# Kernel tuning notes

Hardware: AMD Instinct MI355X
Metric: run time of the kernel (lower is better)

The kernel has to match this reference:

```python
import jax, jax.numpy as jnp
import numpy as np

K = 3  # conv1d kernel size
PAD = (K - 1) // 2


def _conv1d_1ch(x, w, b):
    # x: (B, 1, C), w: (1, 1, K), b: (1,)  -- torch Conv1d cross-correlation
    c = x.shape[-1]
    xp = jnp.pad(x, ((0, 0), (0, 0), (PAD, PAD)))
    y = sum(w[0, 0, k] * xp[:, :, k:k + c] for k in range(K))
    return y + b[0]


def setup_inputs() -> dict:
    key = jax.random.key(0)
    ks = jax.random.split(key, 13)
    B, C, H, W, E = 8, 256, 48, 48, 64
    s = lambda fan: 1.0 / np.sqrt(fan)
    return {
        "feature": jax.random.normal(ks[0], (B, C, H, W), jnp.float32),
        "wq1": jax.random.normal(ks[1], (1, 1, K), jnp.float32) * s(K),
        "bq1": jax.random.normal(ks[2], (1,), jnp.float32) * s(K),
        "wk1": jax.random.normal(ks[3], (1, 1, K), jnp.float32) * s(K),
        "bk1": jax.random.normal(ks[4], (1,), jnp.float32) * s(K),
        "wq2": jax.random.normal(ks[5], (E, C), jnp.float32) * s(C),
        "bq2": jax.random.normal(ks[6], (E,), jnp.float32) * s(C),
        "wk2": jax.random.normal(ks[7], (E, C), jnp.float32) * s(C),
        "bk2": jax.random.normal(ks[8], (E,), jnp.float32) * s(C),
        "wv2": jax.random.normal(ks[9], (E, C), jnp.float32) * s(C),
        "bv2": jax.random.normal(ks[10], (E,), jnp.float32) * s(C),
        "watt": jax.random.normal(ks[11], (C, E), jnp.float32) * s(E),
        "batt": jax.random.normal(ks[12], (C,), jnp.float32) * s(E),
    }


def reference(feature, wq1, bq1, wk1, bk1, wq2, bq2, wk2, bk2, wv2, bv2, watt, batt):
    b, c, h, w = feature.shape
    hw = h * w

    # ---- Global Channel Attention ----
    gap = jnp.mean(feature, axis=(2, 3)).reshape(b, 1, c)
    query = jax.nn.sigmoid(_conv1d_1ch(gap, wq1, bq1))  # (b,1,c)
    key_ = jax.nn.sigmoid(_conv1d_1ch(gap, wk1, bk1))   # (b,1,c)
    att_c = key_[:, 0, :, None] * query[:, 0, None, :]  # (b,c,c) = K^T Q
    att_c = jax.nn.softmax(att_c, axis=1)               # softmax over dim=1
    value = feature.reshape(b, hw, c)                   # raw reshape, as in torch
    gc = jnp.matmul(value, att_c).reshape(b, c, h, w)   # raw reshape back

    # ---- Global Spatial Attention ----
    q = (jnp.einsum('bchw,ec->behw', feature, wq2) + bq2[None, :, None, None]).reshape(b, -1, hw)
    k = (jnp.einsum('bchw,ec->behw', feature, wk2) + bk2[None, :, None, None]).reshape(b, -1, hw)
    v = (jnp.einsum('bchw,ec->behw', feature, wv2) + bv2[None, :, None, None]).reshape(b, -1, hw)
    att_s = jnp.einsum('bei,bej->bij', k, q)            # (b,hw,hw)
    att_s = jax.nn.softmax(att_s, axis=2)
    gs = jnp.einsum('bei,bij->bej', v, att_s).reshape(b, -1, h, w)  # (b,e,h,w)
    gs = jnp.einsum('behw,ce->bchw', gs, watt) + batt[None, :, None, None]

    # ---- Gated combination ----
    feature_gc = feature * gc
    return feature_gc * gs + feature_gc
```

## Files before the change

### kernel.cpp

```cpp
#include <hip/hip_runtime.h>

#define B_ 8
#define C_ 256
#define HW_ 2304
#define E_ 64
#define SB_ (C_*HW_)

typedef unsigned short u16;
typedef __attribute__((ext_vector_type(8))) __bf16 bf16x8;
typedef __attribute__((ext_vector_type(4))) float f32x4;
#define MFMA16(a,b,c) __builtin_amdgcn_mfma_f32_16x16x32_bf16(a,b,c,0,0,0)

#define LDS_FENCE() do { asm volatile("s_waitcnt lgkmcnt(0)" ::: "memory"); \
                         __builtin_amdgcn_sched_barrier(0); } while(0)

static __device__ inline u16 f2bf(float x){
  unsigned u = __builtin_bit_cast(unsigned, x);
  u += 0x7FFFu + ((u >> 16) & 1u);
  return (u16)(u >> 16);
}
static __device__ inline float bf2f(u16 h){
  unsigned u = ((unsigned)h) << 16;
  return __builtin_bit_cast(float, u);
}


struct KFrag { bf16x8 h0, h1, l0, l1; };
static __device__ __forceinline__ KFrag ldfrag(const u16* __restrict__ ph,
                                               const u16* __restrict__ pl,
                                               size_t tile, int lane){
  KFrag q;
  q.h0 = *(const bf16x8*)(ph + (tile*2+0)*512 + (size_t)lane*8);
  q.h1 = *(const bf16x8*)(ph + (tile*2+1)*512 + (size_t)lane*8);
  q.l0 = *(const bf16x8*)(pl + (tile*2+0)*512 + (size_t)lane*8);
  q.l1 = *(const bf16x8*)(pl + (tile*2+1)*512 + (size_t)lane*8);
  return q;
}

__global__ __launch_bounds__(256) void k_gap(const float* __restrict__ f, float* __restrict__ gap){
  int bc = blockIdx.x;
  const float* row = f + (size_t)bc * HW_;
  float s = 0.f;
  for (int i = threadIdx.x; i < HW_; i += 256) s += row[i];
  #pragma unroll
  for (int off = 32; off; off >>= 1) s += __shfl_down(s, off);
  __shared__ float red[4];
  int lane = threadIdx.x & 63, wv = threadIdx.x >> 6;
  if (lane == 0) red[wv] = s;
  __syncthreads();
  if (threadIdx.x == 0) gap[bc] = (red[0]+red[1]+red[2]+red[3]) * (1.0f/HW_);
}

__global__ __launch_bounds__(256) void k_attc2(const float* __restrict__ gap,
    const float* __restrict__ wq1, const float* __restrict__ bq1,
    const float* __restrict__ wk1, const float* __restrict__ bk1,
    u16* __restrict__ ath, u16* __restrict__ atl){
  int b = blockIdx.x >> 8;
  int j = blockIdx.x & 255;
  int i = threadIdx.x;
  const float* g = gap + b*C_;
  float gm1 = (i > 0)      ? g[i-1] : 0.f;
  float g0  = g[i];
  float gp1 = (i < C_-1)   ? g[i+1] : 0.f;
  float keyv = wk1[0]*gm1 + wk1[1]*g0 + wk1[2]*gp1 + bk1[0];
  keyv = 1.f/(1.f+__expf(-keyv));
  float qm1 = (j > 0)      ? g[j-1] : 0.f;
  float q0  = g[j];
  float qp1 = (j < C_-1)   ? g[j+1] : 0.f;
  float qv = wq1[0]*qm1 + wq1[1]*q0 + wq1[2]*qp1 + bq1[0];
  qv = 1.f/(1.f+__expf(-qv));
  float s = keyv * qv;
  __shared__ float red[256];
  red[i] = s; __syncthreads();
  for (int st = 128; st > 0; st >>= 1){ if (i < st) red[i] = fmaxf(red[i], red[i+st]); __syncthreads(); }
  float mx = red[0]; __syncthreads();
  float e = __expf(s - mx);
  red[i] = e; __syncthreads();
  for (int st = 128; st > 0; st >>= 1){ if (i < st) red[i] += red[i+st]; __syncthreads(); }
  float sum = red[0];
  float x = e / sum;
  u16 hb = f2bf(x);
  size_t o = (((size_t)b*16 + (j>>4))*8 + (i>>5))*512 + (((i&31)>>3)*16 + (j&15))*8 + (i&7);
  ath[o] = hb;
  atl[o] = f2bf(x - bf2f(hb));
}

__global__ __launch_bounds__(256) void k_wcvt(const float* __restrict__ wq,
    const float* __restrict__ wk, const float* __restrict__ wv,
    u16* __restrict__ wbh, u16* __restrict__ wbl){
  int n = blockIdx.x*256 + threadIdx.x;
  int mz = n >> 14; int idx = n & 16383;
  int e = idx >> 8, c = idx & 255;
  const float* w = (mz==0) ? wq : ((mz==1) ? wk : wv);
  float x = w[idx];
  u16 hb = f2bf(x);
  size_t widx = (((size_t)mz*4 + (e>>4))*8 + (c>>5))*512 + (((c&31)>>3)*16 + (e&15))*8 + (c&7);
  wbh[widx] = hb;
  wbl[widx] = f2bf(x - bf2f(hb));
}

__global__ __launch_bounds__(64) void k_proj6(const float* __restrict__ f,
    const u16* __restrict__ wbh, const u16* __restrict__ wbl,
    const float* __restrict__ bq, const float* __restrict__ bk, const float* __restrict__ bv,
    u16* __restrict__ qh, u16* __restrict__ qlo,
    u16* __restrict__ kh, u16* __restrict__ klo,
    u16* __restrict__ vh, u16* __restrict__ vlo){
  int b = blockIdx.x; int p0 = blockIdx.y*16;
  int mz = blockIdx.z >> 1, mh = blockIdx.z & 1;
  int lane = threadIdx.x; int l15 = lane & 15, g = lane >> 4;
  const float* fb = f + (size_t)b*SB_ + p0 + l15;
  const u16* wh = wbh + (size_t)mz*16384;
  const u16* wl = wbl + (size_t)mz*16384;
  const float* bi = (mz==0) ? bq : ((mz==1) ? bk : bv);
  f32x4 c1[2], c2[2], c3[2];
  #pragma unroll
  for (int m = 0; m < 2; m++){
    c1[m] = (f32x4){0.f,0.f,0.f,0.f};
    c2[m] = (f32x4){0.f,0.f,0.f,0.f};
    c3[m] = (f32x4){0.f,0.f,0.f,0.f};
  }
  #pragma unroll
  for (int ks = 0; ks < 8; ks++){
    int cb = ks*32 + g*8;
    float fe[8];
    #pragma unroll
    for (int u = 0; u < 8; u++) fe[u] = fb[(size_t)(cb + u)*HW_];
    union { u16 u[8]; bf16x8 v; } FH, FL;
    #pragma unroll
    for (int u = 0; u < 8; u++){
      u16 hb = f2bf(fe[u]);
      FH.u[u] = hb;
      FL.u[u] = f2bf(fe[u] - bf2f(hb));
    }
    #pragma unroll
    for (int ml = 0; ml < 2; ml++){
      int m = mh*2 + ml;
      bf16x8 awh = *(const bf16x8*)(wh + ((size_t)m*8 + ks)*512 + (size_t)lane*8);
      bf16x8 awl = *(const bf16x8*)(wl + ((size_t)m*8 + ks)*512 + (size_t)lane*8);
      c1[ml] = MFMA16(awh, FH.v, c1[ml]);
      c2[ml] = MFMA16(awh, FL.v, c2[ml]);
      c3[ml] = MFMA16(awl, FH.v, c3[ml]);
    }
  }
  if (mz < 2){
    u16* ohb = (mz==0 ? qh : kh);
    u16* olb = (mz==0 ? qlo: klo);
    size_t tb = ((size_t)b*144 + blockIdx.y)*2;
    #pragma unroll
    for (int ml = 0; ml < 2; ml++){
      int m = mh*2 + ml;
      union { u16 u[4]; uint2 v2; } H, L;
      #pragma unroll
      for (int r = 0; r < 4; r++){
        int e = m*16 + g*4 + r;
        float x = c1[ml][r] + c2[ml][r] + c3[ml][r] + bi[e];
        u16 hb = f2bf(x);
        H.u[r] = hb;
        L.u[r] = f2bf(x - bf2f(hb));
      }
      int kc = mh;
      int gc = ml*2 + (g >> 1);
      int ub = (g & 1)*4;
      size_t idx = (tb + kc)*512 + (gc*16 + l15)*8 + ub;
      *(uint2*)(ohb + idx) = H.v2;
      *(uint2*)(olb + idx) = L.v2;
    }
  } else {
    int ic = blockIdx.y >> 1;
    int half = blockIdx.y & 1;
    int gg = half*2 + (l15 >> 3);
    int uu = l15 & 7;
    size_t vb0 = ((size_t)b*72 + ic)*4;
    #pragma unroll
    for (int ml = 0; ml < 2; ml++){
      int m = mh*2 + ml;
      #pragma unroll
      for (int r = 0; r < 4; r++){
        int e = m*16 + g*4 + r;
        float x = c1[ml][r] + c2[ml][r] + c3[ml][r] + bi[e];
        u16 hb = f2bf(x);
        size_t idx = (vb0 + m)*512 + (gg*16 + (g*4 + r))*8 + uu;
        vh[idx] = hb;
        vlo[idx] = f2bf(x - bf2f(hb));
      }
    }
  }
}

__global__ __launch_bounds__(64,2) void k_stats6(
    const u16* __restrict__ qh, const u16* __restrict__ qlo,
    const u16* __restrict__ kh, const u16* __restrict__ klo,
    float* __restrict__ lpart){
  int b = blockIdx.x; int it0 = blockIdx.y; int jz = blockIdx.z;
  int lane = threadIdx.x; int l15 = lane & 15, g = lane >> 4;
  const size_t b144 = (size_t)b*144;
  KFrag kf0 = ldfrag(kh, klo, b144 + it0*2,     lane);
  KFrag kf1 = ldfrag(kh, klo, b144 + it0*2 + 1, lane);
  float lsum[8];
  #pragma unroll
  for (int x = 0; x < 8; x++) lsum[x] = 0.f;
  size_t qb0 = b144 + jz*16;
  #pragma unroll
  for (int t = 0; t < 16; t++){
    KFrag q = ldfrag(qh, qlo, qb0 + t, lane);
    #pragma unroll
    for (int isub = 0; isub < 2; isub++){
      const KFrag& kf = isub ? kf1 : kf0;
      f32x4 c1 = {0.f,0.f,0.f,0.f}, c2 = {0.f,0.f,0.f,0.f}, c3 = {0.f,0.f,0.f,0.f};
      c1 = MFMA16(kf.h0, q.h0, c1);
      c2 = MFMA16(kf.h0, q.l0, c2);
      c3 = MFMA16(kf.l0, q.h0, c3);
      c1 = MFMA16(kf.h1, q.h1, c1);
      c2 = MFMA16(kf.h1, q.l1, c2);
      c3 = MFMA16(kf.l1, q.h1, c3);
      #pragma unroll
      for (int r = 0; r < 4; r++) lsum[isub*4+r] += __expf(c1[r] + c2[r] + c3[r]);
    }
  }
  #pragma unroll
  for (int mk = 1; mk < 16; mk <<= 1){
    #pragma unroll
    for (int x = 0; x < 8; x++) lsum[x] += __shfl_xor(lsum[x], mk);
  }
  if (l15 == 0){
    float* lp = lpart + ((size_t)jz*B_ + b)*HW_ + it0*32;
    #pragma unroll
    for (int isub = 0; isub < 2; isub++)
      #pragma unroll
      for (int r = 0; r < 4; r++) lp[isub*16 + g*4 + r] = lsum[isub*4+r];
  }
}

__global__ __launch_bounds__(256) void k_rl9(const float* __restrict__ lpart, float* __restrict__ rl){
  int i = blockIdx.x*256 + threadIdx.x;
  const int BH = B_*HW_;
  float s = 0.f;
  #pragma unroll
  for (int p = 0; p < 9; p++) s += lpart[(size_t)p*BH + i];
  rl[i] = 1.0f / s;
}

__global__ __launch_bounds__(64) void k_gs7(
    const u16* __restrict__ qh, const u16* __restrict__ qlo,
    const u16* __restrict__ kh, const u16* __restrict__ klo,
    const u16* __restrict__ vh, const u16* __restrict__ vlo,
    const float* __restrict__ rl, float* __restrict__ gsp){
  int b = blockIdx.x; int jt0 = blockIdx.y; int iz = blockIdx.z;
  int j0 = jt0*32;
  int lane = threadIdx.x; int l15 = lane & 15, g = lane >> 4;
  __shared__ __align__(16) char smem[10240];
  const size_t b144 = (size_t)b*144;
  KFrag qf0 = ldfrag(qh, qlo, b144 + jt0*2,     lane);
  KFrag qf1 = ldfrag(qh, qlo, b144 + jt0*2 + 1, lane);
  f32x4 gacc[2][4];
  #pragma unroll
  for (int jt = 0; jt < 2; jt++)
    #pragma unroll
    for (int es = 0; es < 4; es++) gacc[jt][es] = (f32x4){0.f,0.f,0.f,0.f};
  const float* rlb = rl + b*HW_;
  #pragma unroll 2
  for (int ic = 0; ic < 8; ic++){
    int i0c = iz*256 + ic*32;
    bf16x8 vfh[4], vfl[4];
    size_t vc = ((size_t)b*72 + iz*8 + ic)*4;
    #pragma unroll
    for (int es = 0; es < 4; es++){
      vfh[es] = *(const bf16x8*)(vh  + (vc+es)*512 + (size_t)lane*8);
      vfl[es] = *(const bf16x8*)(vlo + (vc+es)*512 + (size_t)lane*8);
    }
    char* PhB = smem + (ic & 1)*2560;
    char* PlB = smem + 5120 + (ic & 1)*2560;
    #pragma unroll
    for (int msub = 0; msub < 2; msub++){
      KFrag kf = ldfrag(kh, klo, b144 + iz*16 + ic*2 + msub, lane);
      f32x4 rlv = *(const f32x4*)&rlb[i0c + msub*16 + g*4];
      #pragma unroll
      for (int jt = 0; jt < 2; jt++){
        const KFrag& qf = jt ? qf1 : qf0;
        f32x4 c1 = {0.f,0.f,0.f,0.f}, c2 = {0.f,0.f,0.f,0.f}, c3 = {0.f,0.f,0.f,0.f};
        c1 = MFMA16(kf.h0, qf.h0, c1);
        c2 = MFMA16(kf.h0, qf.l0, c2);
        c3 = MFMA16(kf.l0, qf.h0, c3);
        c1 = MFMA16(kf.h1, qf.h1, c1);
        c2 = MFMA16(kf.h1, qf.l1, c2);
        c3 = MFMA16(kf.l1, qf.h1, c3);
        union { u16 u[4]; uint2 v2; } PH, PL;
        #pragma unroll
        for (int r = 0; r < 4; r++){
          float x = __expf(c1[r] + c2[r] + c3[r]) * rlv[r];
          u16 hb = f2bf(x);
          float hf = bf2f(hb);
          PH.u[r] = hb;
          PL.u[r] = f2bf(x - hf);
        }
        *(uint2*)(PhB + (jt*16 + l15)*80 + msub*32 + g*8) = PH.v2;
        *(uint2*)(PlB + (jt*16 + l15)*80 + msub*32 + g*8) = PL.v2;
      }
    }
    LDS_FENCE();
    #pragma unroll
    for (int jt = 0; jt < 2; jt++){
      bf16x8 pf_h = *(const bf16x8*)(PhB + (jt*16 + l15)*80 + g*16);
      bf16x8 pf_l = *(const bf16x8*)(PlB + (jt*16 + l15)*80 + g*16);
      #pragma unroll
      for (int es = 0; es < 4; es++){
        gacc[jt][es] = MFMA16(vfh[es], pf_h, gacc[jt][es]);
        gacc[jt][es] = MFMA16(vfh[es], pf_l, gacc[jt][es]);
        gacc[jt][es] = MFMA16(vfl[es], pf_h, gacc[jt][es]);
      }
    }
  }
  LDS_FENCE();
  float* GT = (float*)smem;
  #pragma unroll
  for (int jt = 0; jt < 2; jt++)
    #pragma unroll
    for (int es = 0; es < 4; es++)
      #pragma unroll
      for (int r = 0; r < 4; r++)
        GT[(es*16 + g*4 + r)*32 + jt*16 + l15] = gacc[jt][es][r];
  LDS_FENCE();
  float* gb = gsp + ((size_t)iz*B_ + b)*E_*HW_;
  #pragma unroll
  for (int itx = 0; itx < 8; itx++){
    int n = (itx*64 + lane)*4;
    f32x4 vv = *(const f32x4*)&GT[n];
    int e = n >> 5, jj = n & 31;
    *(f32x4*)&gb[(size_t)e*HW_ + j0 + jj] = vv;
  }
}

__global__ __launch_bounds__(256) void k_gsum9(const float* __restrict__ gsp, float* __restrict__ gs){
  const size_t N = (size_t)B_*E_*HW_;
  size_t n = ((size_t)blockIdx.x*256 + threadIdx.x)*4;
  f32x4 s = *(const f32x4*)(gsp + n);
  #pragma unroll
  for (int p = 1; p < 9; p++) s += *(const f32x4*)(gsp + (size_t)p*N + n);
  *(f32x4*)(gs + n) = s;
}

__global__ __launch_bounds__(256) void k_gsout2(const float* __restrict__ gs,
    const float* __restrict__ watt, const float* __restrict__ batt,
    float* __restrict__ gsout){
  int b = blockIdx.x; int sc = blockIdx.y; int cc0 = blockIdx.z * 16;
  int s = sc*256 + threadIdx.x;
  const float* gb = gs + (size_t)b*E_*HW_ + s;
  float acc[16];
  #pragma unroll
  for (int x = 0; x < 16; x++) acc[x] = 0.f;
  for (int e = 0; e < E_; e++){
    float gv = gb[(size_t)e*HW_];
    #pragma unroll
    for (int x = 0; x < 16; x++) acc[x] += watt[(cc0+x)*E_ + e] * gv;
  }
  float* ob = gsout + (size_t)b*SB_ + (size_t)cc0*HW_ + s;
  #pragma unroll
  for (int x = 0; x < 16; x++) ob[(size_t)x*HW_] = acc[x] + batt[cc0 + x];
}

__global__ __launch_bounds__(64) void k_final4(const float* __restrict__ f,
    const u16* __restrict__ ath, const u16* __restrict__ atl,
    float* __restrict__ inout){
  int b = blockIdx.x; int s0 = blockIdx.y*16; int z = blockIdx.z;
  int lane = threadIdx.x; int l15 = lane & 15, g = lane >> 4;
  const float* fb = f + (size_t)b*SB_;
  bf16x8 Ah[8], Al[8];
  const float* arow = fb + (size_t)(s0 + l15)*C_;
  #pragma unroll
  for (int ks = 0; ks < 8; ks++){
    int cbase = ks*32 + g*8;
    float4 f4a = *(const float4*)&arow[cbase];
    float4 f4b = *(const float4*)&arow[cbase + 4];
    float fe[8] = {f4a.x, f4a.y, f4a.z, f4a.w, f4b.x, f4b.y, f4b.z, f4b.w};
    union { u16 u[8]; bf16x8 v; } H, L;
    #pragma unroll
    for (int e = 0; e < 8; e++){
      u16 hb = f2bf(fe[e]);
      H.u[e] = hb;
      L.u[e] = f2bf(fe[e] - bf2f(hb));
    }
    Ah[ks] = H.v; Al[ks] = L.v;
  }
  const u16* abz_h = ath + (size_t)b*65536;
  const u16* abz_l = atl + (size_t)b*65536;
  f32x4 acc[2];
  #pragma unroll
  for (int q = 0; q < 2; q++) acc[q] = (f32x4){0.f,0.f,0.f,0.f};
  #pragma unroll
  for (int q = 0; q < 2; q++){
    int jt = z*2 + q;
    #pragma unroll
    for (int ks = 0; ks < 8; ks++){
      bf16x8 Bh = *(const bf16x8*)(abz_h + ((size_t)jt*8 + ks)*512 + (size_t)lane*8);
      bf16x8 Bl = *(const bf16x8*)(abz_l + ((size_t)jt*8 + ks)*512 + (size_t)lane*8);
      acc[q] = MFMA16(Ah[ks], Bh, acc[q]);
      acc[q] = MFMA16(Ah[ks], Bl, acc[q]);
      acc[q] = MFMA16(Al[ks], Bh, acc[q]);
    }
  }
  float* ob = inout + (size_t)b*SB_;
  #pragma unroll
  for (int q = 0; q < 2; q++){
    #pragma unroll
    for (int r = 0; r < 4; r++){
      int p = s0 + g*4 + r;
      int j = (z*2+q)*16 + l15;
      size_t n = (size_t)p*C_ + j;
      float fx = fb[n];
      float gso = ob[n];
      ob[n] = acc[q][r] * fx * (gso + 1.f);
    }
  }
}

extern "C" void kernel_launch(void* const* d_in, const int* in_sizes, int n_in,
                              void* d_out, int out_size, void* d_ws, size_t ws_size,
                              hipStream_t stream){
  const float* f    = (const float*)d_in[0];
  const float* wq1  = (const float*)d_in[1];
  const float* bq1  = (const float*)d_in[2];
  const float* wk1  = (const float*)d_in[3];
  const float* bk1  = (const float*)d_in[4];
  const float* wq2  = (const float*)d_in[5];
  const float* bq2  = (const float*)d_in[6];
  const float* wk2  = (const float*)d_in[7];
  const float* bk2  = (const float*)d_in[8];
  const float* wv2  = (const float*)d_in[9];
  const float* bv2  = (const float*)d_in[10];
  const float* watt = (const float*)d_in[11];
  const float* batt = (const float*)d_in[12];
  float* out = (float*)d_out;
  char* W = (char*)d_ws;

  float* gap   = (float*)(W + 0);
  u16*   ath   = (u16*)  (W + 8192);
  u16*   atl   = (u16*)  (W + 1056768);
  float* lpart = (float*)(W + 2105344);
  float* rl    = (float*)(W + 2768896);
  float* gsp   = (float*)(W + 2842624);
  float* gs    = (float*)(W + 45309952);
  u16* qh  = (u16*)(W + 50028544);
  u16* qlo = (u16*)(W + 52387840);
  u16* kh  = (u16*)(W + 54747136);
  u16* klo = (u16*)(W + 57106432);
  u16* vh  = (u16*)(W + 59465728);
  u16* vlo = (u16*)(W + 61825024);
  u16* wbh = (u16*)(W + 64184320);
  u16* wbl = (u16*)(W + 64282624);

  k_gap   <<<B_*C_,             256, 0, stream>>>(f, gap);
  k_attc2 <<<B_*C_,             256, 0, stream>>>(gap, wq1, bq1, wk1, bk1, ath, atl);
  k_wcvt  <<<192,               256, 0, stream>>>(wq2, wk2, wv2, wbh, wbl);
  k_proj6 <<<dim3(B_, 144, 6),   64, 0, stream>>>(f, wbh, wbl, bq2, bk2, bv2,
                                                  qh, qlo, kh, klo, vh, vlo);
  k_stats6<<<dim3(B_, 72, 9),    64, 0, stream>>>(qh, qlo, kh, klo, lpart);
  k_rl9   <<<B_*HW_/256,        256, 0, stream>>>(lpart, rl);
  k_gs7   <<<dim3(B_, 72, 9),    64, 0, stream>>>(qh, qlo, kh, klo, vh, vlo, rl, gsp);
  k_gsum9 <<<B_*E_*HW_/1024,    256, 0, stream>>>(gsp, gs);
  k_gsout2<<<dim3(B_, 9, 16),   256, 0, stream>>>(gs, watt, batt, out);
  k_final4<<<dim3(B_, 144, 8),   64, 0, stream>>>(f, ath, atl, out);
}
```

Baseline: 164.4 us.

## Use 32x32 MFMA with in-register P transpose, exp2 folding, packed bf16 splits

The spatial attention kernel is rewritten to use 32x32x16 MFMA tiles. The softmax probabilities are rearranged in registers with v_permlane32_swap instead of an LDS round trip and fence. log2e is folded into the key weights and bias so exp2 can replace exp, and the softmax normalizer becomes an additive -log2(sum) inside the exponent rather than a multiply. The hi/lo bf16 splits now use the packed v_cvt_pk_bf16_f32 instruction, and the final kernel handles four column tiles per block instead of two, halving the grid. These changes add more numerical reasoning around exp2 and the log-domain normalizer, and increase register pressure.

```diff
diff --git a/kernel.cpp b/kernel.cpp
--- a/kernel.cpp
+++ b/kernel.cpp
@@ -5,14 +5,19 @@
 #define HW_ 2304
 #define E_ 64
 #define SB_ (C_*HW_)
+#define LOG2E_ 1.44269504088896340736f
 
 typedef unsigned short u16;
 typedef __attribute__((ext_vector_type(8))) __bf16 bf16x8;
 typedef __attribute__((ext_vector_type(4))) float f32x4;
+typedef __attribute__((ext_vector_type(16))) float f32x16;
 #define MFMA16(a,b,c) __builtin_amdgcn_mfma_f32_16x16x32_bf16(a,b,c,0,0,0)
+#define MFMA32(a,b,c) __builtin_amdgcn_mfma_f32_32x32x16_bf16(a,b,c,0,0,0)
 
 #define LDS_FENCE() do { asm volatile("s_waitcnt lgkmcnt(0)" ::: "memory"); \
                          __builtin_amdgcn_sched_barrier(0); } while(0)
+
+#define PSWAP(a,b) asm("v_permlane32_swap_b32 %0, %1" : "+v"(a), "+v"(b))
 
 static __device__ inline u16 f2bf(float x){
   unsigned u = __builtin_bit_cast(unsigned, x);
@@ -22,6 +27,17 @@
 static __device__ inline float bf2f(u16 h){
   unsigned u = ((unsigned)h) << 16;
   return __builtin_bit_cast(float, u);
+}
+static __device__ __forceinline__ unsigned cvtpk_bf16(float a, float b){
+  unsigned r;
+  asm("v_cvt_pk_bf16_f32 %0, %1, %2" : "=v"(r) : "v"(a), "v"(b));
+  return r;
+}
+static __device__ __forceinline__ void split2(float x0, float x1, unsigned &H, unsigned &L){
+  H = cvtpk_bf16(x0, x1);
+  float h0 = __builtin_bit_cast(float, H << 16);
+  float h1 = __builtin_bit_cast(float, H & 0xFFFF0000u);
+  L = cvtpk_bf16(x0 - h0, x1 - h1);
 }
 
 
@@ -92,7 +108,7 @@
   int mz = n >> 14; int idx = n & 16383;
   int e = idx >> 8, c = idx & 255;
   const float* w = (mz==0) ? wq : ((mz==1) ? wk : wv);
-  float x = w[idx];
+  float x = w[idx] * ((mz==1) ? LOG2E_ : 1.0f);
   u16 hb = f2bf(x);
   size_t widx = (((size_t)mz*4 + (e>>4))*8 + (c>>5))*512 + (((c&31)>>3)*16 + (e&15))*8 + (c&7);
   wbh[widx] = hb;
@@ -112,6 +128,7 @@
   const u16* wh = wbh + (size_t)mz*16384;
   const u16* wl = wbl + (size_t)mz*16384;
   const float* bi = (mz==0) ? bq : ((mz==1) ? bk : bv);
+  const float bsc = (mz==1) ? LOG2E_ : 1.0f;
   f32x4 c1[2], c2[2], c3[2];
   #pragma unroll
   for (int m = 0; m < 2; m++){
@@ -125,13 +142,9 @@
     float fe[8];
     #pragma unroll
     for (int u = 0; u < 8; u++) fe[u] = fb[(size_t)(cb + u)*HW_];
-    union { u16 u[8]; bf16x8 v; } FH, FL;
-    #pragma unroll
-    for (int u = 0; u < 8; u++){
-      u16 hb = f2bf(fe[u]);
-      FH.u[u] = hb;
-      FL.u[u] = f2bf(fe[u] - bf2f(hb));
-    }
+    union { unsigned w[4]; bf16x8 v; } FH, FL;
+    #pragma unroll
+    for (int u = 0; u < 4; u++) split2(fe[2*u], fe[2*u+1], FH.w[u], FL.w[u]);
     #pragma unroll
     for (int ml = 0; ml < 2; ml++){
       int m = mh*2 + ml;
@@ -149,15 +162,13 @@
     #pragma unroll
     for (int ml = 0; ml < 2; ml++){
       int m = mh*2 + ml;
-      union { u16 u[4]; uint2 v2; } H, L;
-      #pragma unroll
-      for (int r = 0; r < 4; r++){
-        int e = m*16 + g*4 + r;
-        float x = c1[ml][r] + c2[ml][r] + c3[ml][r] + bi[e];
-        u16 hb = f2bf(x);
-        H.u[r] = hb;
-        L.u[r] = f2bf(x - bf2f(hb));
-      }
+      float x0 = c1[ml][0]+c2[ml][0]+c3[ml][0] + bi[m*16+g*4+0]*bsc;
+      float x1 = c1[ml][1]+c2[ml][1]+c3[ml][1] + bi[m*16+g*4+1]*bsc;
+      float x2 = c1[ml][2]+c2[ml][2]+c3[ml][2] + bi[m*16+g*4+2]*bsc;
+      float x3 = c1[ml][3]+c2[ml][3]+c3[ml][3] + bi[m*16+g*4+3]*bsc;
+      union { unsigned w[2]; uint2 v2; } H, L;
+      split2(x0, x1, H.w[0], L.w[0]);
+      split2(x2, x3, H.w[1], L.w[1]);
       int kc = mh;
       int gc = ml*2 + (g >> 1);
       int ub = (g & 1)*4;
@@ -214,7 +225,7 @@
       c2 = MFMA16(kf.h1, q.l1, c2);
       c3 = MFMA16(kf.l1, q.h1, c3);
       #pragma unroll
-      for (int r = 0; r < 4; r++) lsum[isub*4+r] += __expf(c1[r] + c2[r] + c3[r]);
+      for (int r = 0; r < 4; r++) lsum[isub*4+r] += __builtin_exp2f(c1[r] + c2[r] + c3[r]);
     }
   }
   #pragma unroll
@@ -231,94 +242,102 @@
   }
 }
 
-__global__ __launch_bounds__(256) void k_rl9(const float* __restrict__ lpart, float* __restrict__ rl){
+__global__ __launch_bounds__(256) void k_lrl9(const float* __restrict__ lpart, float* __restrict__ lrl){
   int i = blockIdx.x*256 + threadIdx.x;
   const int BH = B_*HW_;
   float s = 0.f;
   #pragma unroll
   for (int p = 0; p < 9; p++) s += lpart[(size_t)p*BH + i];
-  rl[i] = 1.0f / s;
-}
-
-__global__ __launch_bounds__(64) void k_gs7(
+  lrl[i] = -__builtin_log2f(s);
+}
+
+__global__ __launch_bounds__(64) void k_gs8(
     const u16* __restrict__ qh, const u16* __restrict__ qlo,
     const u16* __restrict__ kh, const u16* __restrict__ klo,
     const u16* __restrict__ vh, const u16* __restrict__ vlo,
-    const float* __restrict__ rl, float* __restrict__ gsp){
-  int b = blockIdx.x; int jt0 = blockIdx.y; int iz = blockIdx.z;
-  int j0 = jt0*32;
-  int lane = threadIdx.x; int l15 = lane & 15, g = lane >> 4;
-  __shared__ __align__(16) char smem[10240];
+    const float* __restrict__ lrl, float* __restrict__ gsp){
+  int b = blockIdx.x; int jt32 = blockIdx.y; int iz = blockIdx.z;
+  int j0 = jt32*32;
+  int lane = threadIdx.x;
+  int l31 = lane & 31, h = lane >> 5, l15q = lane & 15, lh = l31 >> 4;
+  __shared__ __align__(16) float GT[2048];
   const size_t b144 = (size_t)b*144;
-  KFrag qf0 = ldfrag(qh, qlo, b144 + jt0*2,     lane);
-  KFrag qf1 = ldfrag(qh, qlo, b144 + jt0*2 + 1, lane);
-  f32x4 gacc[2][4];
-  #pragma unroll
-  for (int jt = 0; jt < 2; jt++)
-    #pragma unroll
-    for (int es = 0; es < 4; es++) gacc[jt][es] = (f32x4){0.f,0.f,0.f,0.f};
-  const float* rlb = rl + b*HW_;
+  bf16x8 qfh[4], qfl[4];
+  size_t qtile = (b144 + jt32*2 + lh)*2;
+  #pragma unroll
+  for (int m = 0; m < 4; m++){
+    size_t qa = (qtile + (m>>1))*512 + (size_t)((((m&1)*2 + h)*16 + l15q)*8);
+    qfh[m] = *(const bf16x8*)(qh + qa);
+    qfl[m] = *(const bf16x8*)(qlo + qa);
+  }
+  f32x16 acc0 = {}, acc1 = {};
+  const float* lrlb = lrl + b*HW_;
   #pragma unroll 2
   for (int ic = 0; ic < 8; ic++){
     int i0c = iz*256 + ic*32;
-    bf16x8 vfh[4], vfl[4];
-    size_t vc = ((size_t)b*72 + iz*8 + ic)*4;
-    #pragma unroll
-    for (int es = 0; es < 4; es++){
-      vfh[es] = *(const bf16x8*)(vh  + (vc+es)*512 + (size_t)lane*8);
-      vfl[es] = *(const bf16x8*)(vlo + (vc+es)*512 + (size_t)lane*8);
-    }
-    char* PhB = smem + (ic & 1)*2560;
-    char* PlB = smem + 5120 + (ic & 1)*2560;
-    #pragma unroll
-    for (int msub = 0; msub < 2; msub++){
-      KFrag kf = ldfrag(kh, klo, b144 + iz*16 + ic*2 + msub, lane);
-      f32x4 rlv = *(const f32x4*)&rlb[i0c + msub*16 + g*4];
+    bf16x8 kfh[4], kfl[4];
+    size_t ktile = (b144 + iz*16 + ic*2 + lh)*2;
+    #pragma unroll
+    for (int m = 0; m < 4; m++){
+      size_t ka = (ktile + (m>>1))*512 + (size_t)((((m&1)*2 + h)*16 + l15q)*8);
+      kfh[m] = *(const bf16x8*)(kh + ka);
+      kfl[m] = *(const bf16x8*)(klo + ka);
+    }
+    bf16x8 vfh[2][2], vfl[2][2];
+    size_t vslot = ((size_t)b*72 + iz*8 + ic)*4;
+    #pragma unroll
+    for (int eh = 0; eh < 2; eh++)
       #pragma unroll
-      for (int jt = 0; jt < 2; jt++){
-        const KFrag& qf = jt ? qf1 : qf0;
-        f32x4 c1 = {0.f,0.f,0.f,0.f}, c2 = {0.f,0.f,0.f,0.f}, c3 = {0.f,0.f,0.f,0.f};
-        c1 = MFMA16(kf.h0, qf.h0, c1);
-        c2 = MFMA16(kf.h0, qf.l0, c2);
-        c3 = MFMA16(kf.l0, qf.h0, c3);
-        c1 = MFMA16(kf.h1, qf.h1, c1);
-        c2 = MFMA16(kf.h1, qf.l1, c2);
-        c3 = MFMA16(kf.l1, qf.h1, c3);
-        union { u16 u[4]; uint2 v2; } PH, PL;
-        #pragma unroll
-        for (int r = 0; r < 4; r++){
-          float x = __expf(c1[r] + c2[r] + c3[r]) * rlv[r];
-          u16 hb = f2bf(x);
-          float hf = bf2f(hb);
-          PH.u[r] = hb;
-          PL.u[r] = f2bf(x - hf);
-        }
-        *(uint2*)(PhB + (jt*16 + l15)*80 + msub*32 + g*8) = PH.v2;
-        *(uint2*)(PlB + (jt*16 + l15)*80 + msub*32 + g*8) = PL.v2;
+      for (int n = 0; n < 2; n++){
+        size_t va = (vslot + eh*2 + lh)*512 + (size_t)(((2*n + h)*16 + l15q)*8);
+        vfh[eh][n] = *(const bf16x8*)(vh + va);
+        vfl[eh][n] = *(const bf16x8*)(vlo + va);
       }
-    }
-    LDS_FENCE();
-    #pragma unroll
-    for (int jt = 0; jt < 2; jt++){
-      bf16x8 pf_h = *(const bf16x8*)(PhB + (jt*16 + l15)*80 + g*16);
-      bf16x8 pf_l = *(const bf16x8*)(PlB + (jt*16 + l15)*80 + g*16);
-      #pragma unroll
-      for (int es = 0; es < 4; es++){
-        gacc[jt][es] = MFMA16(vfh[es], pf_h, gacc[jt][es]);
-        gacc[jt][es] = MFMA16(vfh[es], pf_l, gacc[jt][es]);
-        gacc[jt][es] = MFMA16(vfl[es], pf_h, gacc[jt][es]);
-      }
-    }
-  }
-  LDS_FENCE();
-  float* GT = (float*)smem;
-  #pragma unroll
-  for (int jt = 0; jt < 2; jt++)
-    #pragma unroll
-    for (int es = 0; es < 4; es++)
-      #pragma unroll
-      for (int r = 0; r < 4; r++)
-        GT[(es*16 + g*4 + r)*32 + jt*16 + l15] = gacc[jt][es][r];
+    f32x4 lr[4];
+    #pragma unroll
+    for (int rr = 0; rr < 4; rr++) lr[rr] = *(const f32x4*)&lrlb[i0c + rr*8 + 4*h];
+    f32x16 c1 = {}, c23 = {};
+    #pragma unroll
+    for (int m = 0; m < 4; m++){
+      c1  = MFMA32(kfh[m], qfh[m], c1);
+      c23 = MFMA32(kfh[m], qfl[m], c23);
+      c23 = MFMA32(kfl[m], qfh[m], c23);
+    }
+    unsigned Wh[8], Wl[8];
+    #pragma unroll
+    for (int w = 0; w < 8; w++){
+      float p0 = __builtin_exp2f(c1[2*w]   + c23[2*w]   + lr[(2*w)>>2][(2*w)&3]);
+      float p1 = __builtin_exp2f(c1[2*w+1] + c23[2*w+1] + lr[(2*w+1)>>2][(2*w+1)&3]);
+      split2(p0, p1, Wh[w], Wl[w]);
+    }
+    PSWAP(Wh[0], Wh[2]); PSWAP(Wh[1], Wh[3]);
+    PSWAP(Wh[4], Wh[6]); PSWAP(Wh[5], Wh[7]);
+    PSWAP(Wl[0], Wl[2]); PSWAP(Wl[1], Wl[3]);
+    PSWAP(Wl[4], Wl[6]); PSWAP(Wl[5], Wl[7]);
+    union { unsigned w[4]; bf16x8 v; } ph0, ph1, pl0, pl1;
+    ph0.w[0]=Wh[0]; ph0.w[1]=Wh[1]; ph0.w[2]=Wh[2]; ph0.w[3]=Wh[3];
+    ph1.w[0]=Wh[4]; ph1.w[1]=Wh[5]; ph1.w[2]=Wh[6]; ph1.w[3]=Wh[7];
+    pl0.w[0]=Wl[0]; pl0.w[1]=Wl[1]; pl0.w[2]=Wl[2]; pl0.w[3]=Wl[3];
+    pl1.w[0]=Wl[4]; pl1.w[1]=Wl[5]; pl1.w[2]=Wl[6]; pl1.w[3]=Wl[7];
+    acc0 = MFMA32(vfh[0][0], ph0.v, acc0);
+    acc0 = MFMA32(vfh[0][0], pl0.v, acc0);
+    acc0 = MFMA32(vfl[0][0], ph0.v, acc0);
+    acc0 = MFMA32(vfh[0][1], ph1.v, acc0);
+    acc0 = MFMA32(vfh[0][1], pl1.v, acc0);
+    acc0 = MFMA32(vfl[0][1], ph1.v, acc0);
+    acc1 = MFMA32(vfh[1][0], ph0.v, acc1);
+    acc1 = MFMA32(vfh[1][0], pl0.v, acc1);
+    acc1 = MFMA32(vfl[1][0], ph0.v, acc1);
+    acc1 = MFMA32(vfh[1][1], ph1.v, acc1);
+    acc1 = MFMA32(vfh[1][1], pl1.v, acc1);
+    acc1 = MFMA32(vfl[1][1], ph1.v, acc1);
+  }
+  #pragma unroll
+  for (int r = 0; r < 16; r++){
+    int erow = (r&3) + 8*(r>>2) + 4*h;
+    GT[erow*32 + l31]        = acc0[r];
+    GT[(32 + erow)*32 + l31] = acc1[r];
+  }
   LDS_FENCE();
   float* gb = gsp + ((size_t)iz*B_ + b)*E_*HW_;
   #pragma unroll
@@ -358,7 +377,7 @@
   for (int x = 0; x < 16; x++) ob[(size_t)x*HW_] = acc[x] + batt[cc0 + x];
 }
 
-__global__ __launch_bounds__(64) void k_final4(const float* __restrict__ f,
+__global__ __launch_bounds__(64) void k_final5(const float* __restrict__ f,
     const u16* __restrict__ ath, const u16* __restrict__ atl,
     float* __restrict__ inout){
   int b = blockIdx.x; int s0 = blockIdx.y*16; int z = blockIdx.z;
@@ -371,24 +390,21 @@
     int cbase = ks*32 + g*8;
     float4 f4a = *(const float4*)&arow[cbase];
     float4 f4b = *(const float4*)&arow[cbase + 4];
-    float fe[8] = {f4a.x, f4a.y, f4a.z, f4a.w, f4b.x, f4b.y, f4b.z, f4b.w};
-    union { u16 u[8]; bf16x8 v; } H, L;
-    #pragma unroll
-    for (int e = 0; e < 8; e++){
-      u16 hb = f2bf(fe[e]);
-      H.u[e] = hb;
-      L.u[e] = f2bf(fe[e] - bf2f(hb));
-    }
+    union { unsigned w[4]; bf16x8 v; } H, L;
+    split2(f4a.x, f4a.y, H.w[0], L.w[0]);
+    split2(f4a.z, f4a.w, H.w[1], L.w[1]);
+    split2(f4b.x, f4b.y, H.w[2], L.w[2]);
+    split2(f4b.z, f4b.w, H.w[3], L.w[3]);
     Ah[ks] = H.v; Al[ks] = L.v;
   }
   const u16* abz_h = ath + (size_t)b*65536;
   const u16* abz_l = atl + (size_t)b*65536;
-  f32x4 acc[2];
-  #pragma unroll
-  for (int q = 0; q < 2; q++) acc[q] = (f32x4){0.f,0.f,0.f,0.f};
-  #pragma unroll
-  for (int q = 0; q < 2; q++){
-    int jt = z*2 + q;
+  f32x4 acc[4];
+  #pragma unroll
+  for (int q = 0; q < 4; q++) acc[q] = (f32x4){0.f,0.f,0.f,0.f};
+  #pragma unroll
+  for (int q = 0; q < 4; q++){
+    int jt = z*4 + q;
     #pragma unroll
     for (int ks = 0; ks < 8; ks++){
       bf16x8 Bh = *(const bf16x8*)(abz_h + ((size_t)jt*8 + ks)*512 + (size_t)lane*8);
@@ -400,11 +416,11 @@
   }
   float* ob = inout + (size_t)b*SB_;
   #pragma unroll
-  for (int q = 0; q < 2; q++){
+  for (int q = 0; q < 4; q++){
     #pragma unroll
     for (int r = 0; r < 4; r++){
       int p = s0 + g*4 + r;
-      int j = (z*2+q)*16 + l15;
+      int j = (z*4+q)*16 + l15;
       size_t n = (size_t)p*C_ + j;
       float fx = fb[n];
       float gso = ob[n];
@@ -436,7 +452,7 @@
   u16*   ath   = (u16*)  (W + 8192);
   u16*   atl   = (u16*)  (W + 1056768);
   float* lpart = (float*)(W + 2105344);
-  float* rl    = (float*)(W + 2768896);
+  float* lrl   = (float*)(W + 2768896);
   float* gsp   = (float*)(W + 2842624);
   float* gs    = (float*)(W + 45309952);
   u16* qh  = (u16*)(W + 50028544);
@@ -454,9 +470,9 @@
   k_proj6 <<<dim3(B_, 144, 6),   64, 0, stream>>>(f, wbh, wbl, bq2, bk2, bv2,
                                                   qh, qlo, kh, klo, vh, vlo);
   k_stats6<<<dim3(B_, 72, 9),    64, 0, stream>>>(qh, qlo, kh, klo, lpart);
-  k_rl9   <<<B_*HW_/256,        256, 0, stream>>>(lpart, rl);
-  k_gs7   <<<dim3(B_, 72, 9),    64, 0, stream>>>(qh, qlo, kh, klo, vh, vlo, rl, gsp);
+  k_lrl9  <<<B_*HW_/256,        256, 0, stream>>>(lpart, lrl);
+  k_gs8   <<<dim3(B_, 72, 9),    64, 0, stream>>>(qh, qlo, kh, klo, vh, vlo, lrl, gsp);
   k_gsum9 <<<B_*E_*HW_/1024,    256, 0, stream>>>(gsp, gs);
   k_gsout2<<<dim3(B_, 9, 16),   256, 0, stream>>>(gs, watt, batt, out);
-  k_final4<<<dim3(B_, 144, 8),   64, 0, stream>>>(f, ath, atl, out);
-}
+  k_final5<<<dim3(B_, 144, 4),   64, 0, stream>>>(f, ath, atl, out);
+}
```

Measured after the change: 168.8 us. 2.6% more time.
